# Kernel tuning notes

Hardware: AMD Instinct MI355X
Metric: run time of the kernel (lower is better)

Reference implementation:

```python
import jax, jax.numpy as jnp
import numpy as np

N = 2_000_000
NUM_IN = 9
F1, F2 = 32, 64
NUM_SEG = 100_000
EPS = 1e-5


def setup_inputs() -> dict:
    key = jax.random.key(0)
    ks = jax.random.split(key, 10)
    points = jax.random.normal(ks[0], (N, NUM_IN), dtype=jnp.float32)
    inverse_indices = jax.random.randint(ks[1], (N,), 0, NUM_SEG, dtype=jnp.int64)
    w1 = jax.random.normal(ks[2], (NUM_IN, F1), dtype=jnp.float32) / np.sqrt(NUM_IN)
    b1 = jax.random.normal(ks[3], (F1,), dtype=jnp.float32) * 0.01
    g1 = jnp.ones((F1,), jnp.float32)
    be1 = jnp.zeros((F1,), jnp.float32)
    w2 = jax.random.normal(ks[4], (F1, F2), dtype=jnp.float32) / np.sqrt(F1)
    b2 = jax.random.normal(ks[5], (F2,), dtype=jnp.float32) * 0.01
    g2 = jnp.ones((F2,), jnp.float32)
    be2 = jnp.zeros((F2,), jnp.float32)
    return {
        "points": points, "inverse_indices": inverse_indices, "num_segments": NUM_SEG,
        "w1": w1, "b1": b1, "g1": g1, "be1": be1,
        "w2": w2, "b2": b2, "g2": g2, "be2": be2,
    }


def _linear_bn_relu(x, w, b, gamma, beta):
    # Linear -> BatchNorm1d (training-mode batch stats, biased var, eps=1e-5) -> ReLU
    h = x @ w + b
    mean = h.mean(axis=0)
    var = h.var(axis=0)  # biased, matches torch BN normalization
    h = (h - mean) * jax.lax.rsqrt(var + EPS) * gamma + beta
    return jax.nn.relu(h)


def reference(points, inverse_indices, num_segments, w1, b1, g1, be1, w2, b2, g2, be2):
    feat = _linear_bn_relu(points, w1, b1, g1, be1)
    feat = _linear_bn_relu(feat, w2, b2, g2, be2)
    # scatter_max over dim 0; torch_scatter zero-initializes empty segments,
    # and post-ReLU features are >= 0, so clamp -inf (empty) to 0.
    seg = jax.ops.segment_max(feat, inverse_indices, num_segments=num_segments)
    return jnp.maximum(seg, 0.0)
```

## Files before the change

kernel.cpp:

```cpp
#include <hip/hip_runtime.h>

#define EPS 1e-5f
#define NIN 9
#define F1 32
#define F2 64
#define NMOM 45
#define ROWB 80
#define SHIFT 7
#define NSEGB 128
#define NBMAX 1024
#define BT_BIN 8192
#define WSTRIDE 68

#define WS_S    0
#define WS_M    16
#define WS_S2   64
#define WS_SS2  128
#define WS_SC1  192
#define WS_SH1  224
#define WS_W1P  256
#define WS_SC2  544
#define WS_SH2  608

typedef __attribute__((ext_vector_type(8))) short bf16x8;
typedef __attribute__((ext_vector_type(4))) float f32x4;

__device__ __forceinline__ unsigned int f2bf(float f) {
    unsigned int u = __float_as_uint(f);
    return (u + 0x7fffu + ((u >> 16) & 1u)) >> 16;
}
__device__ __forceinline__ unsigned int pack2(float lo, float hi) {
    unsigned int r;
    asm("v_cvt_pk_bf16_f32 %0, %1, %2" : "=v"(r) : "v"(lo), "v"(hi));
    return r;
}

__device__ __forceinline__ void load_pt9(const float* __restrict__ p, float* __restrict__ x)
{
    const float4* p4 = (const float4*)p;
    const float4 a = p4[0];
    const float4 b = p4[1];
    x[0] = a.x; x[1] = a.y; x[2] = a.z; x[3] = a.w;
    x[4] = b.x; x[5] = b.y; x[6] = b.z; x[7] = b.w;
    x[8] = p[8];
}

#define FOR_S(OP) OP(0) OP(1) OP(2) OP(3) OP(4) OP(5) OP(6) OP(7) OP(8)
#define FOR_M(OP) \
    OP(0,0) OP(0,1) OP(0,2) OP(0,3) OP(0,4) OP(0,5) OP(0,6) OP(0,7) OP(0,8) \
    OP(1,1) OP(1,2) OP(1,3) OP(1,4) OP(1,5) OP(1,6) OP(1,7) OP(1,8) \
    OP(2,2) OP(2,3) OP(2,4) OP(2,5) OP(2,6) OP(2,7) OP(2,8) \
    OP(3,3) OP(3,4) OP(3,5) OP(3,6) OP(3,7) OP(3,8) \
    OP(4,4) OP(4,5) OP(4,6) OP(4,7) OP(4,8) \
    OP(5,5) OP(5,6) OP(5,7) OP(5,8) \
    OP(6,6) OP(6,7) OP(6,8) \
    OP(7,7) OP(7,8) \
    OP(8,8)
#define MIDX(k,l) ((k)*NIN - ((k)*((k)-1))/2 + ((l)-(k)))
#define S_DECL(k)   float S_##k = 0.f;
#define M_DECL(k,l) float M_##k##_##l = 0.f;
#define S_ACC(k)    S_##k += x[k];
#define M_ACC(k,l)  M_##k##_##l = fmaf(x[k], x[l], M_##k##_##l);
#define S_RED(k)    S_##k += __shfl_xor(S_##k, off, 64);
#define M_RED(k,l)  M_##k##_##l += __shfl_xor(M_##k##_##l, off, 64);
#define S_ATM(k)    atomicAdd(&red[WS_S + (k)], S_##k);
#define M_ATM(k,l)  atomicAdd(&red[WS_M + MIDX(k,l)], M_##k##_##l);

__global__ __launch_bounds__(256, 4) void moments_kernel(
    const float* __restrict__ pts, const int* __restrict__ idx,
    float* __restrict__ ws, int* __restrict__ histc, int N, int nb)
{
    __shared__ int lhist[NBMAX];
    __shared__ float red[64];
    for (int t = threadIdx.x; t < nb; t += 256) lhist[t] = 0;

    FOR_S(S_DECL)
    FOR_M(M_DECL)
    __syncthreads();

    const int stride = gridDim.x * blockDim.x;
    for (int i = blockIdx.x * blockDim.x + threadIdx.x; i < N; i += stride) {
        atomicAdd(&lhist[idx[i] >> SHIFT], 1);
        float x[NIN];
        load_pt9(pts + (size_t)i * NIN, x);
        FOR_S(S_ACC)
        FOR_M(M_ACC)
    }
#pragma unroll
    for (int off = 32; off > 0; off >>= 1) {
        FOR_S(S_RED)
        FOR_M(M_RED)
    }
    if (threadIdx.x < 64) red[threadIdx.x] = 0.f;
    __syncthreads();
    if ((threadIdx.x & 63) == 0) {
        FOR_S(S_ATM)
        FOR_M(M_ATM)
    }
    __syncthreads();
    if (threadIdx.x < 64) atomicAdd(&ws[threadIdx.x], red[threadIdx.x]);
    for (int t = threadIdx.x; t < nb; t += 256)
        if (lhist[t] > 0) atomicAdd(&histc[t], lhist[t]);
}

__global__ void scan_coarse_kernel(const int* __restrict__ histc,
                                   int* __restrict__ offsets,
                                   int* __restrict__ cursor, int nb)
{
    __shared__ int part[256];
    const int tid = threadIdx.x;
    int v[4];
    int sum = 0;
    const int base = tid * 4;
#pragma unroll
    for (int j = 0; j < 4; ++j) {
        const int i = base + j;
        v[j] = (i < nb) ? histc[i] : 0;
        sum += v[j];
    }
    part[tid] = sum;
    __syncthreads();
    for (int d = 1; d < 256; d <<= 1) {
        int t = (tid >= d) ? part[tid - d] : 0;
        __syncthreads();
        part[tid] += t;
        __syncthreads();
    }
    int pre = part[tid] - sum;
#pragma unroll
    for (int j = 0; j < 4; ++j) {
        const int i = base + j;
        if (i < nb) { offsets[i] = pre; cursor[i] = pre; }
        pre += v[j];
    }
    if (tid == 255) offsets[nb] = part[255];
}

__global__ void finalize1_kernel(
    const float* __restrict__ w1, const float* __restrict__ b1,
    const float* __restrict__ g1, const float* __restrict__ be1,
    float* __restrict__ ws, float invN)
{
    __shared__ float sc1s[F1];
    const int j = threadIdx.x;
    if (j < F1) {
        float W[NIN];
        float P = 0.f;
#pragma unroll
        for (int k = 0; k < NIN; ++k) {
            W[k] = w1[k * F1 + j];
            P = fmaf(ws[WS_S + k], W[k], P);
        }
        float Q = 0.f;
        int m = 0;
#pragma unroll
        for (int k = 0; k < NIN; ++k) {
            Q = fmaf(ws[WS_M + m], W[k] * W[k], Q); ++m;
#pragma unroll
            for (int l = k + 1; l < NIN; ++l) {
                Q = fmaf(2.f * ws[WS_M + m], W[k] * W[l], Q); ++m;
            }
        }
        const float b = b1[j];
        const float mean = fmaf(P, invN, b);
        const float Eh2 = fmaf(fmaf(2.f * b, P, Q), invN, b * b);
        const float var = Eh2 - mean * mean;
        const float sc = g1[j] * rsqrtf(var + EPS);
        ws[WS_SC1 + j] = sc;
        ws[WS_SH1 + j] = be1[j] - mean * sc;
        sc1s[j] = sc;
    }
    __syncthreads();
    for (int m = threadIdx.x; m < NIN * F1; m += blockDim.x)
        ws[WS_W1P + m] = w1[m] * sc1s[m & (F1 - 1)];
}

__global__ void finalize2_kernel(
    const float* __restrict__ g2, const float* __restrict__ be2,
    const float* __restrict__ b2, float* __restrict__ ws, float invN, float padf)
{
    const int j = threadIdx.x;
    if (j < F2) {
        const float b = b2[j];
        const float S  = ws[WS_S2 + j]  - padf * b;
        const float SS = ws[WS_SS2 + j] - padf * b * b;
        const float mean = S * invN;
        const float var  = SS * invN - mean * mean;
        const float sc   = g2[j] * rsqrtf(var + EPS);
        ws[WS_SC2 + j] = sc;
        ws[WS_SH2 + j] = be2[j] - mean * sc;
    }
}

__device__ __forceinline__ void f1_row_bf16(
    const float* __restrict__ p, const float* __restrict__ wl,
    const float* __restrict__ sh1, unsigned int* __restrict__ pk )
{
    float x[NIN];
    load_pt9(p, x);
#pragma unroll
    for (int fc = 0; fc < 4; ++fc) {
        float h[8];
#pragma unroll
        for (int jj = 0; jj < 8; ++jj) h[jj] = sh1[fc * 8 + jj];
#pragma unroll
        for (int k = 0; k < NIN; ++k) {
            const float xv = x[k];
#pragma unroll
            for (int jj = 0; jj < 8; ++jj)
                h[jj] = fmaf(xv, wl[k * F1 + fc * 8 + jj], h[jj]);
        }
#pragma unroll
        for (int jj = 0; jj < 4; ++jj)
            pk[fc * 4 + jj] = pack2(fmaxf(h[2 * jj], 0.f), fmaxf(h[2 * jj + 1], 0.f));
    }
}

__global__ __launch_bounds__(256, 3) void f1stats_kernel(
    const float* __restrict__ pts, const float* __restrict__ w2,
    const float* __restrict__ b2, float* __restrict__ ws,
    uint4* __restrict__ f1buf, int N)
{
    __shared__ __align__(16) unsigned char stag[4][64 * ROWB];
    __shared__ float red[2 * F2];

    const int lane = threadIdx.x & 63, wv = threadIdx.x >> 6;
    const int quad = lane >> 4, m16 = lane & 15;

    bf16x8 bfr[4];
#pragma unroll
    for (int nt = 0; nt < 4; ++nt)
#pragma unroll
        for (int j = 0; j < 8; ++j)
            bfr[nt][j] = (short)f2bf(w2[(quad * 8 + j) * F2 + nt * 16 + m16]);
    float b2f[4];
#pragma unroll
    for (int nt = 0; nt < 4; ++nt) b2f[nt] = b2[nt * 16 + m16];

    const float* wl  = ws + WS_W1P;
    const float* sh1 = ws + WS_SH1;
    const f32x4 zero = {0.f, 0.f, 0.f, 0.f};
    float s[4] = {0.f, 0.f, 0.f, 0.f}, ss[4] = {0.f, 0.f, 0.f, 0.f};

    unsigned char* myst = stag[wv];
    const int nchunks = (N + 63) / 64;
    for (int c = blockIdx.x * 4 + wv; c < nchunks; c += gridDim.x * 4) {
        const int i = c * 64 + lane;
        unsigned int pk[16];
        if (i < N) {
            f1_row_bf16(pts + (size_t)i * NIN, wl, sh1, pk);
        } else {
#pragma unroll
            for (int q = 0; q < 16; ++q) pk[q] = 0u;
        }
        uint4* wrow = (uint4*)(myst + lane * ROWB);
#pragma unroll
        for (int cidx = 0; cidx < 4; ++cidx)
            wrow[cidx] = make_uint4(pk[4*cidx+0], pk[4*cidx+1], pk[4*cidx+2], pk[4*cidx+3]);

        if (i < N) {
            uint4* dst = f1buf + (size_t)i * 4;
            dst[0] = make_uint4(pk[0],  pk[1],  pk[2],  pk[3]);
            dst[1] = make_uint4(pk[4],  pk[5],  pk[6],  pk[7]);
            dst[2] = make_uint4(pk[8],  pk[9],  pk[10], pk[11]);
            dst[3] = make_uint4(pk[12], pk[13], pk[14], pk[15]);
        }

        bf16x8 afr[4];
#pragma unroll
        for (int mt = 0; mt < 4; ++mt)
            afr[mt] = *(const bf16x8*)(myst + (mt * 16 + m16) * ROWB + quad * 16);
#pragma unroll
        for (int mt = 0; mt < 4; ++mt) {
#pragma unroll
            for (int nt = 0; nt < 4; ++nt) {
                f32x4 d = __builtin_amdgcn_mfma_f32_16x16x32_bf16(afr[mt], bfr[nt], zero, 0, 0, 0);
#pragma unroll
                for (int rr = 0; rr < 4; ++rr) {
                    const float v = d[rr] + b2f[nt];
                    s[nt] += v;
                    ss[nt] = fmaf(v, v, ss[nt]);
                }
            }
        }
    }

#pragma unroll
    for (int off = 16; off < 64; off <<= 1)
#pragma unroll
        for (int nt = 0; nt < 4; ++nt) {
            s[nt]  += __shfl_xor(s[nt], off, 64);
            ss[nt] += __shfl_xor(ss[nt], off, 64);
        }
    if (threadIdx.x < 2 * F2) red[threadIdx.x] = 0.f;
    __syncthreads();
    if (quad == 0) {
#pragma unroll
        for (int nt = 0; nt < 4; ++nt) {
            atomicAdd(&red[nt * 16 + m16], s[nt]);
            atomicAdd(&red[F2 + nt * 16 + m16], ss[nt]);
        }
    }
    __syncthreads();
    if (threadIdx.x < F2) {
        atomicAdd(&ws[WS_S2 + threadIdx.x],  red[threadIdx.x]);
        atomicAdd(&ws[WS_SS2 + threadIdx.x], red[F2 + threadIdx.x]);
    }
}

__global__ __launch_bounds__(256) void binning_kernel(
    const int* __restrict__ idx, int* __restrict__ cursor,
    int2* __restrict__ pair, int N, int nb)
{
    __shared__ int lcnt[NBMAX];
    __shared__ int runbase[NBMAX];
    const int tid = threadIdx.x;
    const int t0 = blockIdx.x * BT_BIN;
    for (int t = tid; t < nb; t += 256) lcnt[t] = 0;
    __syncthreads();
#pragma unroll 4
    for (int r = 0; r < BT_BIN / 256; ++r) {
        const int i = t0 + r * 256 + tid;
        if (i < N) atomicAdd(&lcnt[idx[i] >> SHIFT], 1);
    }
    __syncthreads();
    for (int t = tid; t < nb; t += 256) {
        const int c = lcnt[t];
        if (c > 0) runbase[t] = atomicAdd(&cursor[t], c);
        lcnt[t] = 0;
    }
    __syncthreads();
#pragma unroll 4
    for (int r = 0; r < BT_BIN / 256; ++r) {
        const int i = t0 + r * 256 + tid;
        if (i < N) {
            const int sg = idx[i];
            const int bb = sg >> SHIFT;
            const int p = runbase[bb] + atomicAdd(&lcnt[bb], 1);
            pair[p] = make_int2(i, sg);
        }
    }
}

__global__ __launch_bounds__(256, 3) void bucket_scatter_kernel(
    const uint4* __restrict__ f1buf, const int2* __restrict__ pair,
    const float* __restrict__ w2, const float* __restrict__ b2,
    const float* __restrict__ ws, const int* __restrict__ offsets,
    unsigned int* __restrict__ out, int nseg)
{
    __shared__ unsigned int win[NSEGB * WSTRIDE];
    __shared__ int2 prl[4][64];

    const int b = blockIdx.x;
    const int start = offsets[b], end = offsets[b + 1];
    const int tid = threadIdx.x;
    const int lane = tid & 63, wv = tid >> 6;
    const int quad = lane >> 4, m16 = lane & 15;

    for (int t = tid; t < NSEGB * WSTRIDE; t += 256) win[t] = 0u;

    bf16x8 bfr[4];
#pragma unroll
    for (int nt = 0; nt < 4; ++nt)
#pragma unroll
        for (int j = 0; j < 8; ++j)
            bfr[nt][j] = (short)f2bf(w2[(quad * 8 + j) * F2 + nt * 16 + m16]);
    float sc2f[4], shb[4];
#pragma unroll
    for (int nt = 0; nt < 4; ++nt) {
        const int f = nt * 16 + m16;
        sc2f[nt] = ws[WS_SC2 + f];
        shb[nt]  = fmaf(b2[f], sc2f[nt], ws[WS_SH2 + f]);
    }
    const f32x4 zero = {0.f, 0.f, 0.f, 0.f};
    __syncthreads();

    const int segbase = b << SHIFT;
    const int nch = (end - start + 63) >> 6;
    const bf16x8* fb = (const bf16x8*)f1buf;
    for (int c = wv; c < nch; c += 4) {
        const int cbase = start + c * 64;
        const int sp = cbase + lane;
        int2 pr = make_int2(0, -1);
        if (sp < end) {
            pr = pair[sp];
            pr.y -= segbase;
        }
        prl[wv][lane] = pr;

        bf16x8 afr[4];
#pragma unroll
        for (int mt = 0; mt < 4; ++mt) {
            if (cbase + mt * 16 + m16 < end) {
                const int gi = prl[wv][mt * 16 + m16].x;
                afr[mt] = fb[(size_t)gi * 4 + quad];
            } else {
#pragma unroll
                for (int j = 0; j < 8; ++j) afr[mt][j] = 0;
            }
        }
#pragma unroll
        for (int mt = 0; mt < 4; ++mt) {
            f32x4 d[4];
#pragma unroll
            for (int nt = 0; nt < 4; ++nt)
                d[nt] = __builtin_amdgcn_mfma_f32_16x16x32_bf16(afr[mt], bfr[nt], zero, 0, 0, 0);
#pragma unroll
            for (int rr = 0; rr < 4; ++rr) {
                const int sl = prl[wv][mt * 16 + quad * 4 + rr].y;
                if (sl >= 0) {
#pragma unroll
                    for (int nt = 0; nt < 4; ++nt) {
                        const float v = fmaf(d[nt][rr], sc2f[nt], shb[nt]);
                        if (v > 0.f)
                            atomicMax(&win[sl * WSTRIDE + nt * 16 + m16], __float_as_uint(v));
                    }
                }
            }
        }
    }
    __syncthreads();
    const int rows = min(NSEGB, nseg - segbase);
    for (int t = tid; t < rows * 64; t += 256)
        out[(size_t)(segbase + (t >> 6)) * 64 + (t & 63)] = win[(t >> 6) * WSTRIDE + (t & 63)];
}

__global__ __launch_bounds__(256, 3) void stats2_kernel(
    const float* __restrict__ pts, const float* __restrict__ w2,
    const float* __restrict__ b2, float* __restrict__ ws, int N)
{
    __shared__ __align__(16) unsigned char stag[4][64 * ROWB];
    __shared__ float red[2 * F2];

    const int lane = threadIdx.x & 63, wv = threadIdx.x >> 6;
    const int quad = lane >> 4, m16 = lane & 15;

    bf16x8 bfr[4];
#pragma unroll
    for (int nt = 0; nt < 4; ++nt)
#pragma unroll
        for (int j = 0; j < 8; ++j)
            bfr[nt][j] = (short)f2bf(w2[(quad * 8 + j) * F2 + nt * 16 + m16]);
    float b2f[4];
#pragma unroll
    for (int nt = 0; nt < 4; ++nt) b2f[nt] = b2[nt * 16 + m16];

    const float* wl  = ws + WS_W1P;
    const float* sh1 = ws + WS_SH1;
    const f32x4 zero = {0.f, 0.f, 0.f, 0.f};
    float s[4] = {0.f, 0.f, 0.f, 0.f}, ss[4] = {0.f, 0.f, 0.f, 0.f};

    unsigned char* myst = stag[wv];
    const int nchunks = (N + 63) / 64;
    for (int c = blockIdx.x * 4 + wv; c < nchunks; c += gridDim.x * 4) {
        const int i = c * 64 + lane;
        unsigned int pk[16];
        if (i < N) {
            f1_row_bf16(pts + (size_t)i * NIN, wl, sh1, pk);
        } else {
#pragma unroll
            for (int q = 0; q < 16; ++q) pk[q] = 0u;
        }
        uint4* wrow = (uint4*)(myst + lane * ROWB);
#pragma unroll
        for (int cidx = 0; cidx < 4; ++cidx)
            wrow[cidx] = make_uint4(pk[4*cidx+0], pk[4*cidx+1], pk[4*cidx+2], pk[4*cidx+3]);

        bf16x8 afr[4];
#pragma unroll
        for (int mt = 0; mt < 4; ++mt)
            afr[mt] = *(const bf16x8*)(myst + (mt * 16 + m16) * ROWB + quad * 16);
#pragma unroll
        for (int mt = 0; mt < 4; ++mt) {
#pragma unroll
            for (int nt = 0; nt < 4; ++nt) {
                f32x4 d = __builtin_amdgcn_mfma_f32_16x16x32_bf16(afr[mt], bfr[nt], zero, 0, 0, 0);
#pragma unroll
                for (int rr = 0; rr < 4; ++rr) {
                    const float v = d[rr] + b2f[nt];
                    s[nt] += v;
                    ss[nt] = fmaf(v, v, ss[nt]);
                }
            }
        }
    }
#pragma unroll
    for (int off = 16; off < 64; off <<= 1)
#pragma unroll
        for (int nt = 0; nt < 4; ++nt) {
            s[nt]  += __shfl_xor(s[nt], off, 64);
            ss[nt] += __shfl_xor(ss[nt], off, 64);
        }
    if (threadIdx.x < 2 * F2) red[threadIdx.x] = 0.f;
    __syncthreads();
    if (quad == 0) {
#pragma unroll
        for (int nt = 0; nt < 4; ++nt) {
            atomicAdd(&red[nt * 16 + m16], s[nt]);
            atomicAdd(&red[F2 + nt * 16 + m16], ss[nt]);
        }
    }
    __syncthreads();
    if (threadIdx.x < F2) {
        atomicAdd(&ws[WS_S2 + threadIdx.x],  red[threadIdx.x]);
        atomicAdd(&ws[WS_SS2 + threadIdx.x], red[F2 + threadIdx.x]);
    }
}

__global__ __launch_bounds__(256, 2) void bucket_scatter_gather_kernel(
    const float* __restrict__ pts, const int2* __restrict__ pair,
    const float* __restrict__ w2, const float* __restrict__ b2,
    const float* __restrict__ ws, const int* __restrict__ offsets,
    unsigned int* __restrict__ out, int nseg)
{
    __shared__ unsigned int win[NSEGB * WSTRIDE];
    __shared__ __align__(16) unsigned char stag[4][64 * ROWB];
    __shared__ int segl[4][64];

    const int b = blockIdx.x;
    const int start = offsets[b], end = offsets[b + 1];
    const int tid = threadIdx.x;
    const int lane = tid & 63, wv = tid >> 6;
    const int quad = lane >> 4, m16 = lane & 15;

    for (int t = tid; t < NSEGB * WSTRIDE; t += 256) win[t] = 0u;

    bf16x8 bfr[4];
#pragma unroll
    for (int nt = 0; nt < 4; ++nt)
#pragma unroll
        for (int j = 0; j < 8; ++j)
            bfr[nt][j] = (short)f2bf(w2[(quad * 8 + j) * F2 + nt * 16 + m16]);
    float sc2f[4], shb[4];
#pragma unroll
    for (int nt = 0; nt < 4; ++nt) {
        const int f = nt * 16 + m16;
        sc2f[nt] = ws[WS_SC2 + f];
        shb[nt]  = fmaf(b2[f], sc2f[nt], ws[WS_SH2 + f]);
    }
    const float* wl  = ws + WS_W1P;
    const float* sh1 = ws + WS_SH1;
    const f32x4 zero = {0.f, 0.f, 0.f, 0.f};
    __syncthreads();

    const int segbase = b << SHIFT;
    const int nch = (end - start + 63) >> 6;
    unsigned char* myst = stag[wv];
    for (int c = wv; c < nch; c += 4) {
        const int cbase = start + c * 64;
        const int sp = cbase + lane;
        unsigned int pk[16];
        int sl = -1;
        if (sp < end) {
            const int2 pr = pair[sp];
            f1_row_bf16(pts + (size_t)pr.x * NIN, wl, sh1, pk);
            sl = pr.y - segbase;
        } else {
#pragma unroll
            for (int q = 0; q < 16; ++q) pk[q] = 0u;
        }
        segl[wv][lane] = sl;
        uint4* wrow = (uint4*)(myst + lane * ROWB);
#pragma unroll
        for (int cidx = 0; cidx < 4; ++cidx)
            wrow[cidx] = make_uint4(pk[4*cidx+0], pk[4*cidx+1], pk[4*cidx+2], pk[4*cidx+3]);

        bf16x8 afr[4];
#pragma unroll
        for (int mt = 0; mt < 4; ++mt)
            afr[mt] = *(const bf16x8*)(myst + (mt * 16 + m16) * ROWB + quad * 16);
#pragma unroll
        for (int mt = 0; mt < 4; ++mt) {
            f32x4 d[4];
#pragma unroll
            for (int nt = 0; nt < 4; ++nt)
                d[nt] = __builtin_amdgcn_mfma_f32_16x16x32_bf16(afr[mt], bfr[nt], zero, 0, 0, 0);
#pragma unroll
            for (int rr = 0; rr < 4; ++rr) {
                const int sl2 = segl[wv][mt * 16 + quad * 4 + rr];
                if (sl2 >= 0) {
#pragma unroll
                    for (int nt = 0; nt < 4; ++nt) {
                        const float v = fmaf(d[nt][rr], sc2f[nt], shb[nt]);
                        if (v > 0.f)
                            atomicMax(&win[sl2 * WSTRIDE + nt * 16 + m16], __float_as_uint(v));
                    }
                }
            }
        }
    }
    __syncthreads();
    const int rows = min(NSEGB, nseg - segbase);
    for (int t = tid; t < rows * 64; t += 256)
        out[(size_t)(segbase + (t >> 6)) * 64 + (t & 63)] = win[(t >> 6) * WSTRIDE + (t & 63)];
}

extern "C" void kernel_launch(void* const* d_in, const int* in_sizes, int n_in,
                              void* d_out, int out_size, void* d_ws, size_t ws_size,
                              hipStream_t stream)
{
    const float* pts = (const float*)d_in[0];
    const int*   idx = (const int*)d_in[1];
    const float* w1  = (const float*)d_in[3];
    const float* b1  = (const float*)d_in[4];
    const float* g1  = (const float*)d_in[5];
    const float* be1 = (const float*)d_in[6];
    const float* w2  = (const float*)d_in[7];
    const float* b2  = (const float*)d_in[8];
    const float* g2  = (const float*)d_in[9];
    const float* be2 = (const float*)d_in[10];

    const int N = in_sizes[0] / NIN;
    const int nseg = out_size / F2;
    const int nb = (nseg + NSEGB - 1) >> SHIFT;
    const float invN = 1.0f / (float)N;
    const float padf = (float)((64 - (N & 63)) & 63);

    char* base = (char*)d_ws;
    const size_t f1bytes = (size_t)N * 64;
    const size_t pairbytes = (size_t)N * 8;
    const size_t tailbytes = 4096 + ((size_t)NBMAX + NBMAX + 1 + NBMAX) * sizeof(int) + 256;
    const size_t need_main = f1bytes + pairbytes + tailbytes;

    if (ws_size >= need_main) {
        uint4* f1buf   = (uint4*)base;
        int2*  pair    = (int2*)(base + f1bytes);
        float* ws      = (float*)(base + f1bytes + pairbytes);
        int*   histc   = (int*)(base + f1bytes + pairbytes + 4096);
        int*   offsets = histc + NBMAX;
        int*   cursor  = offsets + NBMAX + 1;

        hipMemsetAsync(ws, 0, 192 * sizeof(float), stream);
        hipMemsetAsync(histc, 0, NBMAX * sizeof(int), stream);

        moments_kernel<<<1024, 256, 0, stream>>>(pts, idx, ws, histc, N, nb);
        finalize1_kernel<<<1, 320, 0, stream>>>(w1, b1, g1, be1, ws, invN);
        scan_coarse_kernel<<<1, 256, 0, stream>>>(histc, offsets, cursor, nb);
        f1stats_kernel<<<1024, 256, 0, stream>>>(pts, w2, b2, ws, f1buf, N);
        binning_kernel<<<(N + BT_BIN - 1) / BT_BIN, 256, 0, stream>>>(
            idx, cursor, pair, N, nb);
        finalize2_kernel<<<1, 64, 0, stream>>>(g2, be2, b2, ws, invN, padf);
        bucket_scatter_kernel<<<nb, 256, 0, stream>>>(
            f1buf, pair, w2, b2, ws, offsets, (unsigned int*)d_out, nseg);
    } else {
        int2*  pair    = (int2*)base;
        float* ws      = (float*)(base + pairbytes);
        int*   histc   = (int*)(base + pairbytes + 4096);
        int*   offsets = histc + NBMAX;
        int*   cursor  = offsets + NBMAX + 1;

        hipMemsetAsync(ws, 0, 192 * sizeof(float), stream);
        hipMemsetAsync(histc, 0, NBMAX * sizeof(int), stream);

        moments_kernel<<<1024, 256, 0, stream>>>(pts, idx, ws, histc, N, nb);
        finalize1_kernel<<<1, 320, 0, stream>>>(w1, b1, g1, be1, ws, invN);
        scan_coarse_kernel<<<1, 256, 0, stream>>>(histc, offsets, cursor, nb);
        binning_kernel<<<(N + BT_BIN - 1) / BT_BIN, 256, 0, stream>>>(
            idx, cursor, pair, N, nb);
        stats2_kernel<<<1024, 256, 0, stream>>>(pts, w2, b2, ws, N);
        finalize2_kernel<<<1, 64, 0, stream>>>(g2, be2, b2, ws, invN, padf);
        bucket_scatter_gather_kernel<<<nb, 256, 0, stream>>>(
            pts, pair, w2, b2, ws, offsets, (unsigned int*)d_out, nseg);
    }
}
```

Before: 308.4 us.

## Replicate global atomic accumulators and split histogram counting out of moments kernel

Global atomic accumulators for input moments, layer-2 stats, and the coarse bucket histogram are now spread over 16 replicas chosen by block index, and the finalize and scan kernels sum the replicas. This is meant to reduce contention from 1024 blocks hitting the same addresses. The histogram counting moves out of the moments kernel into a separate count kernel with fixed-size chunks. That adds an extra launch and a second pass over the index array, and it replaces two memsets with one larger memset.

```diff
diff --git a/kernel.cpp b/kernel.cpp
--- a/kernel.cpp
+++ b/kernel.cpp
@@ -11,11 +11,8 @@
 #define NBMAX 1024
 #define BT_BIN 8192
 #define WSTRIDE 68
-
-#define WS_S    0
-#define WS_M    16
-#define WS_S2   64
-#define WS_SS2  128
+#define NREP 16
+
 #define WS_SC1  192
 #define WS_SH1  224
 #define WS_W1P  256
@@ -63,24 +60,19 @@
 #define M_ACC(k,l)  M_##k##_##l = fmaf(x[k], x[l], M_##k##_##l);
 #define S_RED(k)    S_##k += __shfl_xor(S_##k, off, 64);
 #define M_RED(k,l)  M_##k##_##l += __shfl_xor(M_##k##_##l, off, 64);
-#define S_ATM(k)    atomicAdd(&red[WS_S + (k)], S_##k);
-#define M_ATM(k,l)  atomicAdd(&red[WS_M + MIDX(k,l)], M_##k##_##l);
+#define S_ATM(k)    atomicAdd(&red[(k)], S_##k);
+#define M_ATM(k,l)  atomicAdd(&red[16 + MIDX(k,l)], M_##k##_##l);
 
 __global__ __launch_bounds__(256, 4) void moments_kernel(
-    const float* __restrict__ pts, const int* __restrict__ idx,
-    float* __restrict__ ws, int* __restrict__ histc, int N, int nb)
-{
-    __shared__ int lhist[NBMAX];
+    const float* __restrict__ pts, float* __restrict__ wsrep, int N)
+{
     __shared__ float red[64];
-    for (int t = threadIdx.x; t < nb; t += 256) lhist[t] = 0;
 
     FOR_S(S_DECL)
     FOR_M(M_DECL)
-    __syncthreads();
 
     const int stride = gridDim.x * blockDim.x;
     for (int i = blockIdx.x * blockDim.x + threadIdx.x; i < N; i += stride) {
-        atomicAdd(&lhist[idx[i] >> SHIFT], 1);
         float x[NIN];
         load_pt9(pts + (size_t)i * NIN, x);
         FOR_S(S_ACC)
@@ -98,12 +90,30 @@
         FOR_M(M_ATM)
     }
     __syncthreads();
-    if (threadIdx.x < 64) atomicAdd(&ws[threadIdx.x], red[threadIdx.x]);
-    for (int t = threadIdx.x; t < nb; t += 256)
-        if (lhist[t] > 0) atomicAdd(&histc[t], lhist[t]);
-}
-
-__global__ void scan_coarse_kernel(const int* __restrict__ histc,
+    if (threadIdx.x < 64)
+        atomicAdd(&wsrep[(blockIdx.x & (NREP - 1)) * 64 + threadIdx.x], red[threadIdx.x]);
+}
+
+__global__ __launch_bounds__(256) void count_kernel(
+    const int* __restrict__ idx, int* __restrict__ histcrep, int N, int nb)
+{
+    __shared__ int lhist[NBMAX];
+    const int tid = threadIdx.x;
+    const int t0 = blockIdx.x * BT_BIN;
+    for (int t = tid; t < nb; t += 256) lhist[t] = 0;
+    __syncthreads();
+#pragma unroll 4
+    for (int r = 0; r < BT_BIN / 256; ++r) {
+        const int i = t0 + r * 256 + tid;
+        if (i < N) atomicAdd(&lhist[idx[i] >> SHIFT], 1);
+    }
+    __syncthreads();
+    int* dst = histcrep + (blockIdx.x & (NREP - 1)) * NBMAX;
+    for (int t = tid; t < nb; t += 256)
+        if (lhist[t] > 0) atomicAdd(&dst[t], lhist[t]);
+}
+
+__global__ void scan_coarse_kernel(const int* __restrict__ histcrep,
                                    int* __restrict__ offsets,
                                    int* __restrict__ cursor, int nb)
 {
@@ -115,8 +125,13 @@
 #pragma unroll
     for (int j = 0; j < 4; ++j) {
         const int i = base + j;
-        v[j] = (i < nb) ? histc[i] : 0;
-        sum += v[j];
+        int a = 0;
+        if (i < nb) {
+#pragma unroll
+            for (int r = 0; r < NREP; ++r) a += histcrep[r * NBMAX + i];
+        }
+        v[j] = a;
+        sum += a;
     }
     part[tid] = sum;
     __syncthreads();
@@ -139,26 +154,34 @@
 __global__ void finalize1_kernel(
     const float* __restrict__ w1, const float* __restrict__ b1,
     const float* __restrict__ g1, const float* __restrict__ be1,
-    float* __restrict__ ws, float invN)
+    const float* __restrict__ wsrep, float* __restrict__ ws, float invN)
 {
     __shared__ float sc1s[F1];
+    __shared__ float wsl[64];
     const int j = threadIdx.x;
+    if (j < 64) {
+        float a = 0.f;
+#pragma unroll
+        for (int r = 0; r < NREP; ++r) a += wsrep[r * 64 + j];
+        wsl[j] = a;
+    }
+    __syncthreads();
     if (j < F1) {
         float W[NIN];
         float P = 0.f;
 #pragma unroll
         for (int k = 0; k < NIN; ++k) {
             W[k] = w1[k * F1 + j];
-            P = fmaf(ws[WS_S + k], W[k], P);
+            P = fmaf(wsl[k], W[k], P);
         }
         float Q = 0.f;
         int m = 0;
 #pragma unroll
         for (int k = 0; k < NIN; ++k) {
-            Q = fmaf(ws[WS_M + m], W[k] * W[k], Q); ++m;
+            Q = fmaf(wsl[16 + m], W[k] * W[k], Q); ++m;
 #pragma unroll
             for (int l = k + 1; l < NIN; ++l) {
-                Q = fmaf(2.f * ws[WS_M + m], W[k] * W[l], Q); ++m;
+                Q = fmaf(2.f * wsl[16 + m], W[k] * W[l], Q); ++m;
             }
         }
         const float b = b1[j];
@@ -177,13 +200,20 @@
 
 __global__ void finalize2_kernel(
     const float* __restrict__ g2, const float* __restrict__ be2,
-    const float* __restrict__ b2, float* __restrict__ ws, float invN, float padf)
+    const float* __restrict__ b2, const float* __restrict__ ws2rep,
+    float* __restrict__ ws, float invN, float padf)
 {
     const int j = threadIdx.x;
     if (j < F2) {
+        float S = 0.f, SS = 0.f;
+#pragma unroll
+        for (int r = 0; r < NREP; ++r) {
+            S  += ws2rep[r * 128 + j];
+            SS += ws2rep[r * 128 + 64 + j];
+        }
         const float b = b2[j];
-        const float S  = ws[WS_S2 + j]  - padf * b;
-        const float SS = ws[WS_SS2 + j] - padf * b * b;
+        S  -= padf * b;
+        SS -= padf * b * b;
         const float mean = S * invN;
         const float var  = SS * invN - mean * mean;
         const float sc   = g2[j] * rsqrtf(var + EPS);
@@ -218,8 +248,8 @@
 
 __global__ __launch_bounds__(256, 3) void f1stats_kernel(
     const float* __restrict__ pts, const float* __restrict__ w2,
-    const float* __restrict__ b2, float* __restrict__ ws,
-    uint4* __restrict__ f1buf, int N)
+    const float* __restrict__ b2, const float* __restrict__ ws,
+    float* __restrict__ ws2rep, uint4* __restrict__ f1buf, int N)
 {
     __shared__ __align__(16) unsigned char stag[4][64 * ROWB];
     __shared__ float red[2 * F2];
@@ -302,10 +332,8 @@
         }
     }
     __syncthreads();
-    if (threadIdx.x < F2) {
-        atomicAdd(&ws[WS_S2 + threadIdx.x],  red[threadIdx.x]);
-        atomicAdd(&ws[WS_SS2 + threadIdx.x], red[F2 + threadIdx.x]);
-    }
+    if (threadIdx.x < 2 * F2)
+        atomicAdd(&ws2rep[(blockIdx.x & (NREP - 1)) * 128 + threadIdx.x], red[threadIdx.x]);
 }
 
 __global__ __launch_bounds__(256) void binning_kernel(
@@ -427,7 +455,8 @@
 
 __global__ __launch_bounds__(256, 3) void stats2_kernel(
     const float* __restrict__ pts, const float* __restrict__ w2,
-    const float* __restrict__ b2, float* __restrict__ ws, int N)
+    const float* __restrict__ b2, const float* __restrict__ ws,
+    float* __restrict__ ws2rep, int N)
 {
     __shared__ __align__(16) unsigned char stag[4][64 * ROWB];
     __shared__ float red[2 * F2];
@@ -501,10 +530,8 @@
         }
     }
     __syncthreads();
-    if (threadIdx.x < F2) {
-        atomicAdd(&ws[WS_S2 + threadIdx.x],  red[threadIdx.x]);
-        atomicAdd(&ws[WS_SS2 + threadIdx.x], red[F2 + threadIdx.x]);
-    }
+    if (threadIdx.x < 2 * F2)
+        atomicAdd(&ws2rep[(blockIdx.x & (NREP - 1)) * 128 + threadIdx.x], red[threadIdx.x]);
 }
 
 __global__ __launch_bounds__(256, 2) void bucket_scatter_gather_kernel(
@@ -619,46 +646,53 @@
     char* base = (char*)d_ws;
     const size_t f1bytes = (size_t)N * 64;
     const size_t pairbytes = (size_t)N * 8;
-    const size_t tailbytes = 4096 + ((size_t)NBMAX + NBMAX + 1 + NBMAX) * sizeof(int) + 256;
+    const size_t repbytes = (size_t)NREP * NBMAX * 4 + NREP * 64 * 4 + NREP * 128 * 4;
+    const size_t tailbytes = 4096 + repbytes + ((size_t)NBMAX + 1 + NBMAX) * sizeof(int) + 256;
     const size_t need_main = f1bytes + pairbytes + tailbytes;
 
+    const int nbin = (N + BT_BIN - 1) / BT_BIN;
+
     if (ws_size >= need_main) {
-        uint4* f1buf   = (uint4*)base;
-        int2*  pair    = (int2*)(base + f1bytes);
-        float* ws      = (float*)(base + f1bytes + pairbytes);
-        int*   histc   = (int*)(base + f1bytes + pairbytes + 4096);
-        int*   offsets = histc + NBMAX;
-        int*   cursor  = offsets + NBMAX + 1;
-
-        hipMemsetAsync(ws, 0, 192 * sizeof(float), stream);
-        hipMemsetAsync(histc, 0, NBMAX * sizeof(int), stream);
-
-        moments_kernel<<<1024, 256, 0, stream>>>(pts, idx, ws, histc, N, nb);
-        finalize1_kernel<<<1, 320, 0, stream>>>(w1, b1, g1, be1, ws, invN);
-        scan_coarse_kernel<<<1, 256, 0, stream>>>(histc, offsets, cursor, nb);
-        f1stats_kernel<<<1024, 256, 0, stream>>>(pts, w2, b2, ws, f1buf, N);
-        binning_kernel<<<(N + BT_BIN - 1) / BT_BIN, 256, 0, stream>>>(
-            idx, cursor, pair, N, nb);
-        finalize2_kernel<<<1, 64, 0, stream>>>(g2, be2, b2, ws, invN, padf);
+        uint4* f1buf    = (uint4*)base;
+        int2*  pair     = (int2*)(base + f1bytes);
+        char*  tail     = base + f1bytes + pairbytes;
+        float* ws       = (float*)tail;
+        int*   histcrep = (int*)(tail + 4096);
+        float* wsrep    = (float*)(tail + 4096 + (size_t)NREP * NBMAX * 4);
+        float* ws2rep   = wsrep + NREP * 64;
+        int*   offsets  = (int*)(tail + 4096 + repbytes);
+        int*   cursor   = offsets + NBMAX + 1;
+
+        hipMemsetAsync(histcrep, 0, repbytes, stream);
+
+        moments_kernel<<<1024, 256, 0, stream>>>(pts, wsrep, N);
+        count_kernel<<<nbin, 256, 0, stream>>>(idx, histcrep, N, nb);
+        finalize1_kernel<<<1, 320, 0, stream>>>(w1, b1, g1, be1, wsrep, ws, invN);
+        scan_coarse_kernel<<<1, 256, 0, stream>>>(histcrep, offsets, cursor, nb);
+        f1stats_kernel<<<1024, 256, 0, stream>>>(pts, w2, b2, ws, ws2rep, f1buf, N);
+        binning_kernel<<<nbin, 256, 0, stream>>>(idx, cursor, pair, N, nb);
+        finalize2_kernel<<<1, 64, 0, stream>>>(g2, be2, b2, ws2rep, ws, invN, padf);
         bucket_scatter_kernel<<<nb, 256, 0, stream>>>(
             f1buf, pair, w2, b2, ws, offsets, (unsigned int*)d_out, nseg);
     } else {
-        int2*  pair    = (int2*)base;
-        float* ws      = (float*)(base + pairbytes);
-        int*   histc   = (int*)(base + pairbytes + 4096);
-        int*   offsets = histc + NBMAX;
-        int*   cursor  = offsets + NBMAX + 1;
-
-        hipMemsetAsync(ws, 0, 192 * sizeof(float), stream);
-        hipMemsetAsync(histc, 0, NBMAX * sizeof(int), stream);
-
-        moments_kernel<<<1024, 256, 0, stream>>>(pts, idx, ws, histc, N, nb);
-        finalize1_kernel<<<1, 320, 0, stream>>>(w1, b1, g1, be1, ws, invN);
-        scan_coarse_kernel<<<1, 256, 0, stream>>>(histc, offsets, cursor, nb);
-        binning_kernel<<<(N + BT_BIN - 1) / BT_BIN, 256, 0, stream>>>(
-            idx, cursor, pair, N, nb);
-        stats2_kernel<<<1024, 256, 0, stream>>>(pts, w2, b2, ws, N);
-        finalize2_kernel<<<1, 64, 0, stream>>>(g2, be2, b2, ws, invN, padf);
+        int2*  pair     = (int2*)base;
+        char*  tail     = base + pairbytes;
+        float* ws       = (float*)tail;
+        int*   histcrep = (int*)(tail + 4096);
+        float* wsrep    = (float*)(tail + 4096 + (size_t)NREP * NBMAX * 4);
+        float* ws2rep   = wsrep + NREP * 64;
+        int*   offsets  = (int*)(tail + 4096 + repbytes);
+        int*   cursor   = offsets + NBMAX + 1;
+
+        hipMemsetAsync(histcrep, 0, repbytes, stream);
+
+        moments_kernel<<<1024, 256, 0, stream>>>(pts, wsrep, N);
+        count_kernel<<<nbin, 256, 0, stream>>>(idx, histcrep, N, nb);
+        finalize1_kernel<<<1, 320, 0, stream>>>(w1, b1, g1, be1, wsrep, ws, invN);
+        scan_coarse_kernel<<<1, 256, 0, stream>>>(histcrep, offsets, cursor, nb);
+        binning_kernel<<<nbin, 256, 0, stream>>>(idx, cursor, pair, N, nb);
+        stats2_kernel<<<1024, 256, 0, stream>>>(pts, w2, b2, ws, ws2rep, N);
+        finalize2_kernel<<<1, 64, 0, stream>>>(g2, be2, b2, ws2rep, ws, invN, padf);
         bucket_scatter_gather_kernel<<<nb, 256, 0, stream>>>(
             pts, pair, w2, b2, ws, offsets, (unsigned int*)d_out, nseg);
     }
```

Result: faster. 301.9 us (-2.1%).
